# Kernel tuning notes

Measured on AMD Instinct MI355X. Metric: run time of the kernel, lower is better.

## Reference

```python
import jax, jax.numpy as jnp
import numpy as np

N = 10000      # nodes
E = 320000     # edges (avg degree 32)
D_IN, D_H, D_OUT = 128, 256, 64


def setup_inputs() -> dict:
    key = jax.random.key(0)
    k0, k1, k2, k3 = jax.random.split(key, 4)
    x = jax.random.normal(k0, (N, D_IN), dtype=jnp.float32)
    edge_index = jax.random.randint(k1, (2, E), 0, N, dtype=jnp.int64)
    W1 = jax.random.normal(k2, (D_IN, D_H), dtype=jnp.float32) * 0.05
    b1 = jnp.zeros((D_H,), dtype=jnp.float32)
    W2 = jax.random.normal(k3, (D_H, D_OUT), dtype=jnp.float32) * 0.05
    b2 = jnp.zeros((D_OUT,), dtype=jnp.float32)
    return {"x": x, "edge_index": edge_index, "W1": W1, "b1": b1, "W2": W2, "b2": b2}


def gcn_conv(x, src, dst, W, b, n):
    """PyG GCNConv: linear transform, add self-loops, symmetric D^-1/2 (A+I) D^-1/2 aggregation."""
    h = x @ W                                               # [n, d_out]
    ones = jnp.ones(src.shape[0], dtype=h.dtype)
    deg = jax.ops.segment_sum(ones, dst, num_segments=n) + 1.0  # +1 for self-loop
    dinv = jax.lax.rsqrt(deg)                               # deg^{-1/2}
    norm = (dinv[src] * dinv[dst])[:, None]                 # per-edge coefficient
    agg = jax.ops.segment_sum(h[src] * norm, dst, num_segments=n)
    agg = agg + h * (1.0 / deg)[:, None]                    # self-loop: deg_i^{-1/2}*deg_i^{-1/2}
    return agg + b


def reference(x, edge_index, W1, b1, W2, b2):
    src, dst = edge_index[0], edge_index[1]
    h = jax.nn.relu(gcn_conv(x, src, dst, W1, b1, N))
    z = gcn_conv(h, src, dst, W2, b2, N)                    # [N, D_OUT]
    # decode: pairwise euclidean distance (torch.cdist p=2)
    sq = jnp.sum(z * z, axis=1)                             # [N]
    d2 = sq[:, None] + sq[None, :] - 2.0 * (z @ z.T)        # [N, N]
    d2 = jnp.maximum(d2, 0.0)
    pos = d2 > 0
    dist = jnp.where(pos, jnp.sqrt(jnp.where(pos, d2, 1.0)), 0.0)
    m = jnp.max(dist)
    m = jnp.where(m == 0, jnp.ones((), dist.dtype), m)
    return 1.0 - dist / m
```

## Files before the change

kernel.cpp:

```cpp
#include <hip/hip_runtime.h>
#include <hip/hip_bf16.h>
#include <cstdint>
#include <cstddef>

#define D_IN  128
#define D_H   256
#define D_OUT 64

typedef __attribute__((ext_vector_type(4))) float f32x4;
typedef __attribute__((ext_vector_type(8))) short s16x8;

__global__ void init_k(int* cnt, int* cursor, int* gmax, int n) {
  int i = blockIdx.x * blockDim.x + threadIdx.x;
  int stride = gridDim.x * blockDim.x;
  for (; i < 2 * n + 1; i += stride) {
    if (i < n) cnt[i] = 0;
    else if (i < 2 * n) cursor[i - n] = 0;
    else gmax[0] = 0;
  }
}

__global__ void pad_k(unsigned short* zb, int n, int n_pad) {
  int i = blockIdx.x * blockDim.x + threadIdx.x;
  int total = (n_pad - n) * D_OUT;
  if (i < total) zb[(size_t)n * D_OUT + i] = 0;
}

__global__ void edges_k(const int* __restrict__ raw, int* __restrict__ src,
                        int* __restrict__ dst, int E) {
  __shared__ int flag;
  if (threadIdx.x == 0) {
    int zeros = 0;
    for (int i = 0; i < 64; ++i) zeros += (raw[2 * i + 1] == 0) ? 1 : 0;
    flag = (zeros >= 60) ? 1 : 0;
  }
  __syncthreads();
  int is64 = flag;
  int idx = blockIdx.x * blockDim.x + threadIdx.x;
  int stride = gridDim.x * blockDim.x;
  for (; idx < E; idx += stride) {
    if (is64) {
      src[idx] = raw[2 * idx];
      dst[idx] = raw[2 * (E + idx)];
    } else {
      src[idx] = raw[idx];
      dst[idx] = raw[E + idx];
    }
  }
}

__global__ void count_k(const int* __restrict__ dst, int* cnt, int E) {
  int idx = blockIdx.x * blockDim.x + threadIdx.x;
  int stride = gridDim.x * blockDim.x;
  for (; idx < E; idx += stride) atomicAdd(&cnt[dst[idx]], 1);
}

__global__ void deg_k(const int* __restrict__ cnt, float* __restrict__ dinv, int n) {
  int i = blockIdx.x * blockDim.x + threadIdx.x;
  if (i < n) dinv[i] = rsqrtf((float)cnt[i] + 1.0f);
}

__global__ void scan_k(const int* __restrict__ cnt, int* __restrict__ offs, int n) {
  __shared__ int sums[1024];
  int t = threadIdx.x;
  const int CH = 10;
  int base = t * CH;
  int local[CH];
  int s = 0;
  for (int i = 0; i < CH; ++i) {
    int v = (base + i < n) ? cnt[base + i] : 0;
    local[i] = s;
    s += v;
  }
  sums[t] = s;
  __syncthreads();
  for (int off = 1; off < 1024; off <<= 1) {
    int v = (t >= off) ? sums[t - off] : 0;
    __syncthreads();
    sums[t] += v;
    __syncthreads();
  }
  int prefix = (t > 0) ? sums[t - 1] : 0;
  for (int i = 0; i < CH; ++i)
    if (base + i < n) offs[base + i] = prefix + local[i];
  if (t == 1023) offs[n] = sums[1023];
}

__global__ void fill_k(const int* __restrict__ src, const int* __restrict__ dst,
                       const int* __restrict__ offs, int* __restrict__ cursor,
                       const float* __restrict__ dinv, int* __restrict__ csr_src,
                       float* __restrict__ csr_norm, int E) {
  int idx = blockIdx.x * blockDim.x + threadIdx.x;
  int stride = gridDim.x * blockDim.x;
  for (; idx < E; idx += stride) {
    int d = dst[idx], s = src[idx];
    int pos = atomicAdd(&cursor[d], 1);
    int slot = offs[d] + pos;
    csr_src[slot] = s;
    csr_norm[slot] = dinv[s] * dinv[d];
  }
}

__global__ void gemm_k(const float* __restrict__ A, const float* __restrict__ B,
                       float* __restrict__ C, int M, int N, int K) {
  __shared__ float As[16][64];
  __shared__ float Bs[16][64];
  int t = threadIdx.x;
  int bm = blockIdx.x * 64, bn = blockIdx.y * 64;
  int tx = t & 15, ty = t >> 4;
  int lr = t >> 2;
  int lk = (t & 3) * 4;
  int br = t >> 4;
  int bc = (t & 15) * 4;
  float acc[4][4] = {};
  for (int k0 = 0; k0 < K; k0 += 16) {
    float4 av = make_float4(0.f, 0.f, 0.f, 0.f);
    if (bm + lr < M) av = *(const float4*)&A[(size_t)(bm + lr) * K + k0 + lk];
    As[lk + 0][lr] = av.x;
    As[lk + 1][lr] = av.y;
    As[lk + 2][lr] = av.z;
    As[lk + 3][lr] = av.w;
    float4 bv = *(const float4*)&B[(size_t)(k0 + br) * N + bn + bc];
    *(float4*)&Bs[br][bc] = bv;
    __syncthreads();
#pragma unroll
    for (int k = 0; k < 16; ++k) {
      float4 a = *(const float4*)&As[k][ty * 4];
      float4 b = *(const float4*)&Bs[k][tx * 4];
      acc[0][0] += a.x * b.x; acc[0][1] += a.x * b.y; acc[0][2] += a.x * b.z; acc[0][3] += a.x * b.w;
      acc[1][0] += a.y * b.x; acc[1][1] += a.y * b.y; acc[1][2] += a.y * b.z; acc[1][3] += a.y * b.w;
      acc[2][0] += a.z * b.x; acc[2][1] += a.z * b.y; acc[2][2] += a.z * b.z; acc[2][3] += a.z * b.w;
      acc[3][0] += a.w * b.x; acc[3][1] += a.w * b.y; acc[3][2] += a.w * b.z; acc[3][3] += a.w * b.w;
    }
    __syncthreads();
  }
  for (int r = 0; r < 4; ++r) {
    int row = bm + ty * 4 + r;
    if (row < M)
      *(float4*)&C[(size_t)row * N + bn + tx * 4] =
          make_float4(acc[r][0], acc[r][1], acc[r][2], acc[r][3]);
  }
}

__global__ void agg1_k(const float* __restrict__ h, const int* __restrict__ offs,
                       const int* __restrict__ csr_src, const float* __restrict__ csr_norm,
                       const float* __restrict__ dinv, const float* __restrict__ b1,
                       float* __restrict__ h1, int n) {
  int wid = blockIdx.x * 4 + (threadIdx.x >> 6);
  int lane = threadIdx.x & 63;
  if (wid >= n) return;
  float di = dinv[wid];
  float selfw = di * di;
  float4 acc = *(const float4*)&b1[lane * 4];
  float4 hv = *(const float4*)&h[(size_t)wid * D_H + lane * 4];
  acc.x += hv.x * selfw; acc.y += hv.y * selfw; acc.z += hv.z * selfw; acc.w += hv.w * selfw;
  int e0 = offs[wid], e1 = offs[wid + 1];
  for (int e = e0; e < e1; ++e) {
    int s = csr_src[e];
    float w = csr_norm[e];
    float4 v = *(const float4*)&h[(size_t)s * D_H + lane * 4];
    acc.x += v.x * w; acc.y += v.y * w; acc.z += v.z * w; acc.w += v.w * w;
  }
  acc.x = fmaxf(acc.x, 0.f); acc.y = fmaxf(acc.y, 0.f);
  acc.z = fmaxf(acc.z, 0.f); acc.w = fmaxf(acc.w, 0.f);
  *(float4*)&h1[(size_t)wid * D_H + lane * 4] = acc;
}

__global__ void agg2_k(const float* __restrict__ h2, const int* __restrict__ offs,
                       const int* __restrict__ csr_src, const float* __restrict__ csr_norm,
                       const float* __restrict__ dinv, const float* __restrict__ b2,
                       unsigned short* __restrict__ zb, float* __restrict__ sq, int n) {
  int wid = blockIdx.x * 4 + (threadIdx.x >> 6);
  int lane = threadIdx.x & 63;
  if (wid >= n) return;
  float di = dinv[wid];
  float selfw = di * di;
  float acc = b2[lane] + h2[(size_t)wid * D_OUT + lane] * selfw;
  int e0 = offs[wid], e1 = offs[wid + 1];
  for (int e = e0; e < e1; ++e) {
    int s = csr_src[e];
    float w = csr_norm[e];
    acc += h2[(size_t)s * D_OUT + lane] * w;
  }
  unsigned u = __float_as_uint(acc);
  unsigned rb = (u + 0x7fffu + ((u >> 16) & 1u)) >> 16;
  zb[(size_t)wid * D_OUT + lane] = (unsigned short)rb;
  float back = __uint_as_float(rb << 16);
  float ss = back * back;
#pragma unroll
  for (int o = 32; o > 0; o >>= 1) ss += __shfl_xor(ss, o, 64);
  if (lane == 0) sq[wid] = ss;
}

__global__ __launch_bounds__(256, 1) void decode_mfma_k(
    const unsigned short* __restrict__ zb, const float* __restrict__ sq,
    float* __restrict__ out, float* __restrict__ blockmax,
    const int* __restrict__ gmax, int n, int mode) {
  __shared__ __align__(16) char ZiB[128 * 128];
  __shared__ __align__(16) char ZjB[128 * 128];
  __shared__ float sqi[128];
  __shared__ float sqj[128];
  __shared__ float wmax[4];
  int t = threadIdx.x;
  int i0 = blockIdx.y * 128, j0 = blockIdx.x * 128;

#pragma unroll
  for (int it = 0; it < 4; ++it) {
    int c = t + it * 256;
    int row = c >> 3, s = c & 7;
    int dstb = row * 128 + ((s * 16) ^ ((row & 7) << 4));
    s16x8 vi = *(const s16x8*)&zb[(size_t)(i0 + row) * D_OUT + s * 8];
    *(s16x8*)&ZiB[dstb] = vi;
    s16x8 vj = *(const s16x8*)&zb[(size_t)(j0 + row) * D_OUT + s * 8];
    *(s16x8*)&ZjB[dstb] = vj;
  }
  if (t < 128) sqi[t] = (i0 + t < n) ? sq[i0 + t] : 0.f;
  else { int tt = t - 128; sqj[tt] = (j0 + tt < n) ? sq[j0 + tt] : 0.f; }
  __syncthreads();

  int lane = t & 63;
  int wid = t >> 6;
  int wr = (wid >> 1) * 64;
  int wc = (wid & 1) * 64;
  int lrow = lane & 15;
  int lgrp = lane >> 4;
  int swz = (lrow & 7) << 4;

  f32x4 acc[4][4] = {};
#pragma unroll
  for (int ks = 0; ks < 2; ++ks) {
    s16x8 a[4], b[4];
    int kb = (ks * 64) ^ (lgrp * 16) ^ swz;
#pragma unroll
    for (int q = 0; q < 4; ++q) {
      a[q] = *(const s16x8*)&ZiB[(wr + q * 16 + lrow) * 128 + kb];
      b[q] = *(const s16x8*)&ZjB[(wc + q * 16 + lrow) * 128 + kb];
    }
#pragma unroll
    for (int rt = 0; rt < 4; ++rt)
#pragma unroll
      for (int ct = 0; ct < 4; ++ct)
        acc[rt][ct] = __builtin_amdgcn_mfma_f32_16x16x32_bf16(a[rt], b[ct], acc[rt][ct], 0, 0, 0);
  }

  float sqa[4][4], sqb[4];
#pragma unroll
  for (int rt = 0; rt < 4; ++rt)
#pragma unroll
    for (int reg = 0; reg < 4; ++reg)
      sqa[rt][reg] = sqi[wr + rt * 16 + lgrp * 4 + reg];
#pragma unroll
  for (int ct = 0; ct < 4; ++ct) sqb[ct] = sqj[wc + ct * 16 + lrow];

  if (mode == 0) {
    float lmax = 0.f;
#pragma unroll
    for (int rt = 0; rt < 4; ++rt)
#pragma unroll
      for (int ct = 0; ct < 4; ++ct)
#pragma unroll
        for (int reg = 0; reg < 4; ++reg) {
          int i = i0 + wr + rt * 16 + lgrp * 4 + reg;
          int j = j0 + wc + ct * 16 + lrow;
          if (i < n && j < n) {
            float d2 = sqa[rt][reg] + sqb[ct] - 2.f * acc[rt][ct][reg];
            lmax = fmaxf(lmax, d2);
          }
        }
#pragma unroll
    for (int o = 32; o > 0; o >>= 1) lmax = fmaxf(lmax, __shfl_xor(lmax, o, 64));
    if (lane == 0) wmax[wid] = lmax;
    __syncthreads();
    if (t == 0) {
      float m = fmaxf(fmaxf(wmax[0], wmax[1]), fmaxf(wmax[2], wmax[3]));
      blockmax[blockIdx.y * gridDim.x + blockIdx.x] = m;
    }
  } else {
    float m2 = __int_as_float(*gmax);
    float inv = (m2 > 0.f) ? (1.f / m2) : 0.f;
#pragma unroll
    for (int rt = 0; rt < 4; ++rt)
#pragma unroll
      for (int reg = 0; reg < 4; ++reg) {
        int i = i0 + wr + rt * 16 + lgrp * 4 + reg;
        if (i >= n) continue;
        size_t rowbase = (size_t)i * n;
#pragma unroll
        for (int ct = 0; ct < 4; ++ct) {
          int j = j0 + wc + ct * 16 + lrow;
          if (j >= n) continue;
          float d2 = sqa[rt][reg] + sqb[ct] - 2.f * acc[rt][ct][reg];
          out[rowbase + j] = (d2 > 0.f) ? (1.f - sqrtf(d2 * inv)) : 1.f;
        }
      }
  }
}

__global__ void reduce_k(const float* __restrict__ bm, int* __restrict__ gmax, int nb) {
  __shared__ float s[1024];
  int t = threadIdx.x;
  float m = 0.f;
  for (int i = t; i < nb; i += 1024) m = fmaxf(m, bm[i]);
  s[t] = m;
  __syncthreads();
  for (int o = 512; o > 0; o >>= 1) {
    if (t < o) s[t] = fmaxf(s[t], s[t + o]);
    __syncthreads();
  }
  if (t == 0) gmax[0] = __float_as_int(s[0]);
}

extern "C" void kernel_launch(void* const* d_in, const int* in_sizes, int n_in,
                              void* d_out, int out_size, void* d_ws, size_t ws_size,
                              hipStream_t stream) {
  const float* x  = (const float*)d_in[0];
  const int* eraw = (const int*)d_in[1];
  const float* W1 = (const float*)d_in[2];
  const float* b1 = (const float*)d_in[3];
  const float* W2 = (const float*)d_in[4];
  const float* b2 = (const float*)d_in[5];
  float* out = (float*)d_out;

  const int n = in_sizes[0] / D_IN;
  const int E = in_sizes[1] / 2;
  const int gt = (n + 127) / 128;
  const int n_pad = gt * 128;

  char* p = (char*)d_ws;
  auto alloc = [&](size_t bytes) {
    void* r = (void*)p;
    p += (bytes + 255) & ~(size_t)255;
    return r;
  };
  int*   cnt      = (int*)alloc((size_t)n * 4);
  int*   offs     = (int*)alloc((size_t)(n + 1) * 4);
  int*   cursor   = (int*)alloc((size_t)n * 4);
  int*   esrc     = (int*)alloc((size_t)E * 4);
  int*   edst     = (int*)alloc((size_t)E * 4);
  int*   csr_src  = (int*)alloc((size_t)E * 4);
  float* csr_norm = (float*)alloc((size_t)E * 4);
  float* dinv     = (float*)alloc((size_t)n * 4);
  float* h        = (float*)alloc((size_t)n * D_H * 4);
  float* h1       = (float*)alloc((size_t)n * D_H * 4);
  float* h2       = (float*)alloc((size_t)n * D_OUT * 4);
  unsigned short* zbuf = (unsigned short*)alloc((size_t)n_pad * D_OUT * 2);
  float* sq       = (float*)alloc((size_t)n * 4);
  float* blockmax = (float*)alloc((size_t)gt * gt * 4);
  int*   gmax     = (int*)alloc(4);

  init_k<<<64, 256, 0, stream>>>(cnt, cursor, gmax, n);
  pad_k<<<((n_pad - n) * D_OUT + 255) / 256, 256, 0, stream>>>(zbuf, n, n_pad);
  edges_k<<<512, 256, 0, stream>>>(eraw, esrc, edst, E);
  count_k<<<512, 256, 0, stream>>>(edst, cnt, E);
  deg_k<<<(n + 255) / 256, 256, 0, stream>>>(cnt, dinv, n);
  scan_k<<<1, 1024, 0, stream>>>(cnt, offs, n);
  fill_k<<<512, 256, 0, stream>>>(esrc, edst, offs, cursor, dinv, csr_src, csr_norm, E);

  gemm_k<<<dim3((n + 63) / 64, D_H / 64), 256, 0, stream>>>(x, W1, h, n, D_H, D_IN);
  agg1_k<<<(n + 3) / 4, 256, 0, stream>>>(h, offs, csr_src, csr_norm, dinv, b1, h1, n);

  gemm_k<<<dim3((n + 63) / 64, D_OUT / 64), 256, 0, stream>>>(h1, W2, h2, n, D_OUT, D_H);
  agg2_k<<<(n + 3) / 4, 256, 0, stream>>>(h2, offs, csr_src, csr_norm, dinv, b2, zbuf, sq, n);

  decode_mfma_k<<<dim3(gt, gt), 256, 0, stream>>>(zbuf, sq, out, blockmax, gmax, n, 0);
  reduce_k<<<1, 1024, 0, stream>>>(blockmax, gmax, gt * gt);
  decode_mfma_k<<<dim3(gt, gt), 256, 0, stream>>>(zbuf, sq, out, blockmax, gmax, n, 1);
}
```

Measured before the change: 305.3 us.

## Fuse prep kernels, store layer-1 features as bf16, exploit symmetry in max pass

Merges the init, pad and edge-conversion kernels into one launch and folds the degree/rsqrt computation into the scan kernel. The first GEMM now writes bf16 so the gather in the first aggregation moves half the bytes. The second GEMM gets a dedicated 32-row tile kernel for the 64-wide output, and the max-distance pass runs only on upper-triangular tile pairs because the distance matrix is symmetric. The cost is lower precision on the first-layer features, which could move the output slightly away from the float reference.

```diff
diff --git a/kernel.cpp b/kernel.cpp
--- a/kernel.cpp
+++ b/kernel.cpp
@@ -10,24 +10,18 @@
 typedef __attribute__((ext_vector_type(4))) float f32x4;
 typedef __attribute__((ext_vector_type(8))) short s16x8;
 
-__global__ void init_k(int* cnt, int* cursor, int* gmax, int n) {
-  int i = blockIdx.x * blockDim.x + threadIdx.x;
-  int stride = gridDim.x * blockDim.x;
-  for (; i < 2 * n + 1; i += stride) {
-    if (i < n) cnt[i] = 0;
-    else if (i < 2 * n) cursor[i - n] = 0;
-    else gmax[0] = 0;
-  }
-}
-
-__global__ void pad_k(unsigned short* zb, int n, int n_pad) {
-  int i = blockIdx.x * blockDim.x + threadIdx.x;
-  int total = (n_pad - n) * D_OUT;
-  if (i < total) zb[(size_t)n * D_OUT + i] = 0;
-}
-
-__global__ void edges_k(const int* __restrict__ raw, int* __restrict__ src,
-                        int* __restrict__ dst, int E) {
+__device__ __forceinline__ unsigned short f2bf(float f) {
+  unsigned u = __float_as_uint(f);
+  return (unsigned short)((u + 0x7fffu + ((u >> 16) & 1u)) >> 16);
+}
+__device__ __forceinline__ float bf2f(unsigned short b) {
+  return __uint_as_float(((unsigned)b) << 16);
+}
+
+__global__ void prep_k(const int* __restrict__ raw, int* __restrict__ cnt,
+                       int* __restrict__ cursor, int* __restrict__ gmax,
+                       unsigned short* __restrict__ zb, int* __restrict__ src,
+                       int* __restrict__ dst, int n, int npadElems, int E) {
   __shared__ int flag;
   if (threadIdx.x == 0) {
     int zeros = 0;
@@ -36,15 +30,17 @@
   }
   __syncthreads();
   int is64 = flag;
+  int T = n + 1 + npadElems + E;
   int idx = blockIdx.x * blockDim.x + threadIdx.x;
   int stride = gridDim.x * blockDim.x;
-  for (; idx < E; idx += stride) {
-    if (is64) {
-      src[idx] = raw[2 * idx];
-      dst[idx] = raw[2 * (E + idx)];
-    } else {
-      src[idx] = raw[idx];
-      dst[idx] = raw[E + idx];
+  for (; idx < T; idx += stride) {
+    if (idx < n) { cnt[idx] = 0; cursor[idx] = 0; }
+    else if (idx == n) gmax[0] = 0;
+    else if (idx < n + 1 + npadElems) zb[(size_t)n * D_OUT + (idx - (n + 1))] = 0;
+    else {
+      int e = idx - (n + 1 + npadElems);
+      if (is64) { src[e] = raw[2 * e]; dst[e] = raw[2 * (E + e)]; }
+      else      { src[e] = raw[e];     dst[e] = raw[E + e]; }
     }
   }
 }
@@ -55,12 +51,8 @@
   for (; idx < E; idx += stride) atomicAdd(&cnt[dst[idx]], 1);
 }
 
-__global__ void deg_k(const int* __restrict__ cnt, float* __restrict__ dinv, int n) {
-  int i = blockIdx.x * blockDim.x + threadIdx.x;
-  if (i < n) dinv[i] = rsqrtf((float)cnt[i] + 1.0f);
-}
-
-__global__ void scan_k(const int* __restrict__ cnt, int* __restrict__ offs, int n) {
+__global__ void scan_k(const int* __restrict__ cnt, int* __restrict__ offs,
+                       float* __restrict__ dinv, int n) {
   __shared__ int sums[1024];
   int t = threadIdx.x;
   const int CH = 10;
@@ -69,6 +61,7 @@
   int s = 0;
   for (int i = 0; i < CH; ++i) {
     int v = (base + i < n) ? cnt[base + i] : 0;
+    if (base + i < n) dinv[base + i] = rsqrtf((float)v + 1.0f);
     local[i] = s;
     s += v;
   }
@@ -101,8 +94,8 @@
   }
 }
 
-__global__ void gemm_k(const float* __restrict__ A, const float* __restrict__ B,
-                       float* __restrict__ C, int M, int N, int K) {
+__global__ void gemm1_k(const float* __restrict__ A, const float* __restrict__ B,
+                        unsigned short* __restrict__ C, int M, int N, int K) {
   __shared__ float As[16][64];
   __shared__ float Bs[16][64];
   int t = threadIdx.x;
@@ -136,30 +129,73 @@
   }
   for (int r = 0; r < 4; ++r) {
     int row = bm + ty * 4 + r;
+    if (row < M) {
+      ushort4 o;
+      o.x = f2bf(acc[r][0]); o.y = f2bf(acc[r][1]);
+      o.z = f2bf(acc[r][2]); o.w = f2bf(acc[r][3]);
+      *(ushort4*)&C[(size_t)row * N + bn + tx * 4] = o;
+    }
+  }
+}
+
+__global__ void gemm2_k(const float* __restrict__ A, const float* __restrict__ B,
+                        float* __restrict__ C, int M, int N, int K) {
+  __shared__ float As[16][32];
+  __shared__ float Bs[16][64];
+  int t = threadIdx.x;
+  int bm = blockIdx.x * 32;
+  int tx = t & 15, ty = t >> 4;
+  int lr = t >> 3;
+  int lkk = (t & 7) * 2;
+  int br = t >> 4;
+  int bc = (t & 15) * 4;
+  float acc[2][4] = {};
+  for (int k0 = 0; k0 < K; k0 += 16) {
+    float2 av = make_float2(0.f, 0.f);
+    if (bm + lr < M) av = *(const float2*)&A[(size_t)(bm + lr) * K + k0 + lkk];
+    As[lkk + 0][lr] = av.x;
+    As[lkk + 1][lr] = av.y;
+    float4 bv = *(const float4*)&B[(size_t)(k0 + br) * N + bc];
+    *(float4*)&Bs[br][bc] = bv;
+    __syncthreads();
+#pragma unroll
+    for (int k = 0; k < 16; ++k) {
+      float a0 = As[k][ty * 2], a1 = As[k][ty * 2 + 1];
+      float4 b = *(const float4*)&Bs[k][tx * 4];
+      acc[0][0] += a0 * b.x; acc[0][1] += a0 * b.y; acc[0][2] += a0 * b.z; acc[0][3] += a0 * b.w;
+      acc[1][0] += a1 * b.x; acc[1][1] += a1 * b.y; acc[1][2] += a1 * b.z; acc[1][3] += a1 * b.w;
+    }
+    __syncthreads();
+  }
+  for (int r = 0; r < 2; ++r) {
+    int row = bm + ty * 2 + r;
     if (row < M)
-      *(float4*)&C[(size_t)row * N + bn + tx * 4] =
+      *(float4*)&C[(size_t)row * N + tx * 4] =
           make_float4(acc[r][0], acc[r][1], acc[r][2], acc[r][3]);
   }
 }
 
-__global__ void agg1_k(const float* __restrict__ h, const int* __restrict__ offs,
+__global__ void agg1_k(const unsigned short* __restrict__ hb, const int* __restrict__ offs,
                        const int* __restrict__ csr_src, const float* __restrict__ csr_norm,
                        const float* __restrict__ dinv, const float* __restrict__ b1,
                        float* __restrict__ h1, int n) {
   int wid = blockIdx.x * 4 + (threadIdx.x >> 6);
   int lane = threadIdx.x & 63;
   if (wid >= n) return;
+  const ushort4* hb4 = (const ushort4*)hb;
   float di = dinv[wid];
   float selfw = di * di;
   float4 acc = *(const float4*)&b1[lane * 4];
-  float4 hv = *(const float4*)&h[(size_t)wid * D_H + lane * 4];
-  acc.x += hv.x * selfw; acc.y += hv.y * selfw; acc.z += hv.z * selfw; acc.w += hv.w * selfw;
+  ushort4 sv = hb4[(size_t)wid * 64 + lane];
+  acc.x += bf2f(sv.x) * selfw; acc.y += bf2f(sv.y) * selfw;
+  acc.z += bf2f(sv.z) * selfw; acc.w += bf2f(sv.w) * selfw;
   int e0 = offs[wid], e1 = offs[wid + 1];
   for (int e = e0; e < e1; ++e) {
     int s = csr_src[e];
     float w = csr_norm[e];
-    float4 v = *(const float4*)&h[(size_t)s * D_H + lane * 4];
-    acc.x += v.x * w; acc.y += v.y * w; acc.z += v.z * w; acc.w += v.w * w;
+    ushort4 v = hb4[(size_t)s * 64 + lane];
+    acc.x += bf2f(v.x) * w; acc.y += bf2f(v.y) * w;
+    acc.z += bf2f(v.z) * w; acc.w += bf2f(v.w) * w;
   }
   acc.x = fmaxf(acc.x, 0.f); acc.y = fmaxf(acc.y, 0.f);
   acc.z = fmaxf(acc.z, 0.f); acc.w = fmaxf(acc.w, 0.f);
@@ -182,10 +218,9 @@
     float w = csr_norm[e];
     acc += h2[(size_t)s * D_OUT + lane] * w;
   }
-  unsigned u = __float_as_uint(acc);
-  unsigned rb = (u + 0x7fffu + ((u >> 16) & 1u)) >> 16;
-  zb[(size_t)wid * D_OUT + lane] = (unsigned short)rb;
-  float back = __uint_as_float(rb << 16);
+  unsigned short rb = f2bf(acc);
+  zb[(size_t)wid * D_OUT + lane] = rb;
+  float back = bf2f(rb);
   float ss = back * back;
 #pragma unroll
   for (int o = 32; o > 0; o >>= 1) ss += __shfl_xor(ss, o, 64);
@@ -202,7 +237,19 @@
   __shared__ float sqj[128];
   __shared__ float wmax[4];
   int t = threadIdx.x;
-  int i0 = blockIdx.y * 128, j0 = blockIdx.x * 128;
+
+  int bi, bj;
+  if (mode == 0) {
+    int b = blockIdx.x;
+    int tj = (int)((sqrtf(8.f * (float)b + 1.f) - 1.f) * 0.5f);
+    while ((tj + 1) * (tj + 2) / 2 <= b) ++tj;
+    while (tj * (tj + 1) / 2 > b) --tj;
+    bj = tj;
+    bi = b - tj * (tj + 1) / 2;
+  } else {
+    bi = blockIdx.y; bj = blockIdx.x;
+  }
+  int i0 = bi * 128, j0 = bj * 128;
 
 #pragma unroll
   for (int it = 0; it < 4; ++it) {
@@ -273,7 +320,7 @@
     __syncthreads();
     if (t == 0) {
       float m = fmaxf(fmaxf(wmax[0], wmax[1]), fmaxf(wmax[2], wmax[3]));
-      blockmax[blockIdx.y * gridDim.x + blockIdx.x] = m;
+      blockmax[blockIdx.x] = m;
     }
   } else {
     float m2 = __int_as_float(*gmax);
@@ -325,6 +372,7 @@
   const int E = in_sizes[1] / 2;
   const int gt = (n + 127) / 128;
   const int n_pad = gt * 128;
+  const int nbU = gt * (gt + 1) / 2;
 
   char* p = (char*)d_ws;
   auto alloc = [&](size_t bytes) {
@@ -340,29 +388,29 @@
   int*   csr_src  = (int*)alloc((size_t)E * 4);
   float* csr_norm = (float*)alloc((size_t)E * 4);
   float* dinv     = (float*)alloc((size_t)n * 4);
-  float* h        = (float*)alloc((size_t)n * D_H * 4);
+  unsigned short* hb = (unsigned short*)alloc((size_t)n * D_H * 2);
   float* h1       = (float*)alloc((size_t)n * D_H * 4);
   float* h2       = (float*)alloc((size_t)n * D_OUT * 4);
   unsigned short* zbuf = (unsigned short*)alloc((size_t)n_pad * D_OUT * 2);
   float* sq       = (float*)alloc((size_t)n * 4);
-  float* blockmax = (float*)alloc((size_t)gt * gt * 4);
+  float* blockmax = (float*)alloc((size_t)nbU * 4);
   int*   gmax     = (int*)alloc(4);
 
-  init_k<<<64, 256, 0, stream>>>(cnt, cursor, gmax, n);
-  pad_k<<<((n_pad - n) * D_OUT + 255) / 256, 256, 0, stream>>>(zbuf, n, n_pad);
-  edges_k<<<512, 256, 0, stream>>>(eraw, esrc, edst, E);
+  const int npadElems = (n_pad - n) * D_OUT;
+  const int prepT = n + 1 + npadElems + E;
+  prep_k<<<(prepT + 255) / 256, 256, 0, stream>>>(eraw, cnt, cursor, gmax, zbuf,
+                                                  esrc, edst, n, npadElems, E);
   count_k<<<512, 256, 0, stream>>>(edst, cnt, E);
-  deg_k<<<(n + 255) / 256, 256, 0, stream>>>(cnt, dinv, n);
-  scan_k<<<1, 1024, 0, stream>>>(cnt, offs, n);
+  scan_k<<<1, 1024, 0, stream>>>(cnt, offs, dinv, n);
   fill_k<<<512, 256, 0, stream>>>(esrc, edst, offs, cursor, dinv, csr_src, csr_norm, E);
 
-  gemm_k<<<dim3((n + 63) / 64, D_H / 64), 256, 0, stream>>>(x, W1, h, n, D_H, D_IN);
-  agg1_k<<<(n + 3) / 4, 256, 0, stream>>>(h, offs, csr_src, csr_norm, dinv, b1, h1, n);
-
-  gemm_k<<<dim3((n + 63) / 64, D_OUT / 64), 256, 0, stream>>>(h1, W2, h2, n, D_OUT, D_H);
+  gemm1_k<<<dim3((n + 63) / 64, D_H / 64), 256, 0, stream>>>(x, W1, hb, n, D_H, D_IN);
+  agg1_k<<<(n + 3) / 4, 256, 0, stream>>>(hb, offs, csr_src, csr_norm, dinv, b1, h1, n);
+
+  gemm2_k<<<(n + 31) / 32, 256, 0, stream>>>(h1, W2, h2, n, D_OUT, D_H);
   agg2_k<<<(n + 3) / 4, 256, 0, stream>>>(h2, offs, csr_src, csr_norm, dinv, b2, zbuf, sq, n);
 
-  decode_mfma_k<<<dim3(gt, gt), 256, 0, stream>>>(zbuf, sq, out, blockmax, gmax, n, 0);
-  reduce_k<<<1, 1024, 0, stream>>>(blockmax, gmax, gt * gt);
+  decode_mfma_k<<<nbU, 256, 0, stream>>>(zbuf, sq, out, blockmax, gmax, n, 0);
+  reduce_k<<<1, 1024, 0, stream>>>(blockmax, gmax, nbU);
   decode_mfma_k<<<dim3(gt, gt), 256, 0, stream>>>(zbuf, sq, out, blockmax, gmax, n, 1);
 }
```

New measurement: 275.5 us. 1.11x faster.
